# Kernel optimization log

Measured on AMD Instinct MI355X. Metric: run time of the kernel, lower is better.

The kernel has to match this reference:

```python
import jax, jax.numpy as jnp
import numpy as np

B, T_ENC, E, T_DEC, N_MELS, H, A = 32, 256, 512, 200, 80, 1024, 128


def setup_inputs() -> dict:
    key = jax.random.key(0)
    ks = jax.random.split(key, 20)
    rn = lambda k, s, sc: (jax.random.normal(k, s, jnp.float32) * sc)
    return {
        "inputs": rn(ks[0], (B, T_ENC, E), 1.0),
        "padded_mels": rn(ks[1], (B, N_MELS, T_DEC), 1.0),
        "W_enc": rn(ks[2], (E, A), 0.04),
        "W_q": rn(ks[3], (H, A), 0.03),
        "conv_w": rn(ks[4], (32, 1, 31), 0.18),
        "conv_b": jnp.zeros((32,), jnp.float32),
        "W_loc": rn(ks[5], (32, A), 0.18),
        "v_e": rn(ks[6], (A,), 0.09),
        "pw1": rn(ks[7], (N_MELS, 256), 0.11),
        "pb1": jnp.zeros((256,), jnp.float32),
        "pw2": rn(ks[8], (256, 256), 0.06),
        "pb2": jnp.zeros((256,), jnp.float32),
        "Wi1": rn(ks[9], (256 + E, 4 * H), 0.03),
        "Wh1": rn(ks[10], (H, 4 * H), 0.03),
        "bl1": jnp.zeros((4 * H,), jnp.float32),
        "Wi2": rn(ks[11], (H, 4 * H), 0.03),
        "Wh2": rn(ks[12], (H, 4 * H), 0.03),
        "bl2": jnp.zeros((4 * H,), jnp.float32),
        "Wp": rn(ks[13], (H + E, N_MELS), 0.025),
        "bp": jnp.zeros((N_MELS,), jnp.float32),
    }


def _lstm_cell(x, h, c, Wi, Wh, b):
    g = x @ Wi + h @ Wh + b
    i, f, gg, o = jnp.split(g, 4, axis=-1)
    c = jax.nn.sigmoid(f) * c + jax.nn.sigmoid(i) * jnp.tanh(gg)
    h = jax.nn.sigmoid(o) * jnp.tanh(c)
    return h, c


def reference(inputs, padded_mels, W_enc, W_q, conv_w, conv_b, W_loc, v_e,
              pw1, pb1, pw2, pb2, Wi1, Wh1, bl1, Wi2, Wh2, bl2, Wp, bp):
    b, t_enc, e = inputs.shape
    n_mels, t_dec = padded_mels.shape[1], padded_mels.shape[2]
    proc_enc = inputs @ W_enc  # [B, T_enc, A]
    # teacher forcing: prepend go frame, use frames 0..T_dec-1 as inputs
    go = jnp.zeros((b, n_mels, 1), inputs.dtype)
    prev_mels = jnp.moveaxis(jnp.concatenate([go, padded_mels], axis=-1)[:, :, :-1], -1, 0)  # [T_dec,B,80]

    def step(carry, prev_mel):
        h1, c1, h2, c2, ctx, aw_cum = carry
        # prenet (dropout omitted: eval/deterministic reference)
        x = jax.nn.relu(prev_mel @ pw1 + pb1)
        x = jax.nn.relu(x @ pw2 + pb2)
        # 2-layer LSTM on [prenet, prev context]
        lstm_in = jnp.concatenate([x, ctx], axis=-1)
        h1n, c1n = _lstm_cell(lstm_in, h1, c1, Wi1, Wh1, bl1)
        h2n, c2n = _lstm_cell(h1n, h2, c2, Wi2, Wh2, bl2)
        # location-sensitive attention
        q = h2n @ W_q  # [B, A]
        loc = jax.lax.conv_general_dilated(aw_cum[:, None, :], conv_w, (1,), "SAME",
                                           dimension_numbers=("NCH", "OIH", "NCH"))
        loc = loc + conv_b[None, :, None]
        loc = jnp.swapaxes(loc, 1, 2) @ W_loc  # [B, T_enc, A]
        energies = jnp.tanh(q[:, None, :] + loc + proc_enc) @ v_e  # [B, T_enc]
        aw = jax.nn.softmax(energies, axis=1)
        ctx_n = jnp.einsum("bt,bte->be", aw, inputs)
        out = jnp.concatenate([h2n, ctx_n], axis=-1) @ Wp + bp  # [B, 80]
        return (h1n, c1n, h2n, c2n, ctx_n, aw_cum + aw), out

    z = lambda *s: jnp.zeros(s, inputs.dtype)
    carry0 = (z(b, H), z(b, H), z(b, H), z(b, H), z(b, e), z(b, t_enc))
    _, mels = jax.lax.scan(step, carry0, prev_mels)
    return mels  # [T_dec, B, 80]
```

## Files before the change

### kernel.cpp

```cpp
#include <hip/hip_runtime.h>
#include <hip/hip_fp16.h>

#define BB   32
#define TENC 256
#define EE   512
#define TDEC 200
#define NM   80
#define HH   1024
#define AA   128
#define GG   4096
#define K1   1792
#define K2   2048

#define NGRP  16
#define GRPSZ 16

typedef _Float16 h8v  __attribute__((ext_vector_type(8)));
typedef float    f32x4 __attribute__((ext_vector_type(4)));

__device__ __forceinline__ float sigf(float x){ return 1.0f/(1.0f + __expf(-x)); }
__device__ __forceinline__ float tanhfast(float x){ return 1.0f - 2.0f/(1.0f + __expf(2.0f*x)); }

__device__ __forceinline__ unsigned short h2b(float f){
    _Float16 h = (_Float16)f; unsigned short u; __builtin_memcpy(&u, &h, 2); return u;
}
__device__ __forceinline__ void st64(unsigned long long* p, unsigned long long v){
    __hip_atomic_store(p, v, __ATOMIC_RELAXED, __HIP_MEMORY_SCOPE_AGENT);
}
__device__ __forceinline__ void st32(unsigned int* p, unsigned int v){
    __hip_atomic_store(p, v, __ATOMIC_RELAXED, __HIP_MEMORY_SCOPE_AGENT);
}
__device__ __forceinline__ unsigned long long ld64(const unsigned long long* p){
    return __hip_atomic_load(p, __ATOMIC_RELAXED, __HIP_MEMORY_SCOPE_AGENT);
}
__device__ __forceinline__ unsigned int ld32(const unsigned int* p){
    return __hip_atomic_load(p, __ATOMIC_RELAXED, __HIP_MEMORY_SCOPE_AGENT);
}


__global__ void k_zero(float* __restrict__ p, int n){
    int i = blockIdx.x*blockDim.x + threadIdx.x;
    if(i < n) p[i] = 0.f;
}

__global__ void k_cvt_half(const float* __restrict__ src, __half* __restrict__ dst, int n){
    int i = blockIdx.x*blockDim.x + threadIdx.x;
    int stride = gridDim.x*blockDim.x;
    for(; i<n; i+=stride) dst[i] = __float2half(src[i]);
}

__global__ __launch_bounds__(256) void k_transpose2(const float* __restrict__ src,
                                                    _Float16* __restrict__ dst,
                                                    int K, int C, int dstStride, int kOff, int pack){
    __shared__ float tile[32][33];
    const int tid = threadIdx.x;
    const int c0 = blockIdx.x*32, k0 = blockIdx.y*32;
    const int cl = tid & 31, r8 = tid >> 5;
    #pragma unroll
    for(int i=0;i<4;i++){
        const int k = k0 + r8 + i*8;
        if(k < K && c0+cl < C) tile[r8 + i*8][cl] = src[(size_t)k*C + c0 + cl];
    }
    __syncthreads();
    const int kl = tid & 31, c8 = tid >> 5;
    #pragma unroll
    for(int i=0;i<4;i++){
        const int c = c0 + c8 + i*8;
        if(c < C && k0+kl < K){
            const int p = pack ? ((c & 1023)*4 + (c >> 10)) : c;
            dst[(size_t)p*dstStride + kOff + k0 + kl] = (_Float16)tile[kl][c8 + i*8];
        }
    }
}

__global__ __launch_bounds__(256) void k_wfrag(const _Float16* __restrict__ WT,
                                               _Float16* __restrict__ WF, int K){
    const int tid = threadIdx.x;
    const int l = tid & 63, f = tid >> 6;
    const int ct = blockIdx.y;
    const int kc = blockIdx.x*4 + f;
    const h8v v = *(const h8v*)(WT + (size_t)(ct*16 + (l & 15))*K + kc*32 + ((l >> 4) << 3));
    *(h8v*)(WF + ((size_t)(ct*(K >> 5) + kc)*64 + l)*8) = v;
}

__global__ __launch_bounds__(128) void k_proc_enc(const float* __restrict__ inputs,
                                                  const float* __restrict__ Wenc,
                                                  __half* __restrict__ pe_h){
    const int row = blockIdx.x;
    const int a   = threadIdx.x;
    const float* in = inputs + (size_t)row*EE;
    float acc = 0.f;
    for(int k=0;k<EE;k++) acc = fmaf(in[k], Wenc[k*AA + a], acc);
    pe_h[(size_t)row*AA + a] = __float2half(acc);
}

__global__ __launch_bounds__(320) void k_pip(const float* __restrict__ inputs,
                                             const float* __restrict__ Wp_c,
                                             __half* __restrict__ PIP){
    const int b = blockIdx.x >> 6, t4 = (blockIdx.x & 63)*4;
    __shared__ float xs[4*EE];
    const int tid = threadIdx.x;
    for(int i=tid; i<4*EE; i+=320) xs[i] = inputs[((size_t)b*TENC + t4)*EE + i];
    __syncthreads();
    const int tl = tid/80, m = tid%80;
    float acc = 0.f;
    for(int k=0;k<EE;k++) acc = fmaf(xs[tl*EE + k], Wp_c[k*NM + m], acc);
    PIP[((size_t)b*TENC + t4 + tl)*NM + m] = __float2half(acc);
}

__global__ __launch_bounds__(256) void k_prenet(const float* __restrict__ pmels,
                                                const float* __restrict__ pw1, const float* __restrict__ pb1,
                                                const float* __restrict__ pw2, const float* __restrict__ pb2,
                                                _Float16* __restrict__ XS1h){
    const int t = blockIdx.x;
    __shared__ float pm[BB*NM];
    __shared__ float h1s[BB*256];
    const int tid = threadIdx.x;
    for(int el=tid; el<BB*NM; el+=256){
        const int b = el/NM, m = el%NM;
        pm[el] = (t==0) ? 0.f : pmels[(size_t)(b*NM + m)*TDEC + (t-1)];
    }
    __syncthreads();
    const int a = tid;
    float acc[BB];
    #pragma unroll
    for(int b=0;b<BB;b++) acc[b]=0.f;
    for(int m=0;m<NM;m++){
        const float w = pw1[m*256 + a];
        #pragma unroll
        for(int b=0;b<BB;b++) acc[b] = fmaf(pm[b*NM+m], w, acc[b]);
    }
    {
        const float bias = pb1[a];
        for(int b=0;b<BB;b++) h1s[b*256+a] = fmaxf(acc[b]+bias, 0.f);
    }
    __syncthreads();
    #pragma unroll
    for(int b=0;b<BB;b++) acc[b]=0.f;
    for(int k=0;k<256;k++){
        const float w = pw2[k*256 + a];
        #pragma unroll
        for(int b=0;b<BB;b++) acc[b] = fmaf(h1s[b*256+k], w, acc[b]);
    }
    {
        const float bias = pb2[a];
        #pragma unroll
        for(int b=0;b<BB;b++)
            XS1h[((size_t)t*BB + b)*K1 + a] = (_Float16)fmaxf(acc[b]+bias, 0.f);
    }
}

__global__ void k_mloc(const float* __restrict__ conv_w, const float* __restrict__ conv_b,
                       const float* __restrict__ W_loc, float* __restrict__ Mloc, float* __restrict__ cbp){
    const int a = threadIdx.x;
    for(int d=0; d<31; d++){
        float s = 0.f;
        for(int ch=0; ch<32; ch++) s = fmaf(conv_w[ch*31 + d], W_loc[ch*AA + a], s);
        Mloc[d*AA + a] = s;
    }
    float s = 0.f;
    for(int ch=0; ch<32; ch++) s = fmaf(conv_b[ch], W_loc[ch*AA + a], s);
    cbp[a] = s;
}


__device__ __forceinline__ void gridbar(unsigned int* bb, unsigned int bi, int tid, int bid, int& dead){
    __syncthreads();
    if(tid == 0){
        const int g = bid >> 4;
        unsigned int v = __hip_atomic_fetch_add(&bb[g*32], 1u, __ATOMIC_RELAXED, __HIP_MEMORY_SCOPE_AGENT);
        if(v == bi*GRPSZ - 1u){
            unsigned int w = __hip_atomic_fetch_add(&bb[512], 1u, __ATOMIC_RELAXED, __HIP_MEMORY_SCOPE_AGENT);
            if(w == bi*NGRP - 1u)
                st32(&bb[544], bi);
        }
        if(!dead){
            unsigned int guard = 0;
            if((bid & 15) == 0){
                while(ld32(&bb[544]) < bi){
                    __builtin_amdgcn_s_sleep(4);
                    if(++guard > 3000000u){ dead = 1; break; }
                }
                #pragma unroll
                for(int m=1; m<GRPSZ; m++) st32(&bb[576 + (bid+m)*32], bi);
            } else {
                while(ld32(&bb[576 + bid*32]) < bi){
                    __builtin_amdgcn_s_sleep(4);
                    if(++guard > 3000000u){ dead = 1; break; }
                }
            }
        }
    }
    __syncthreads();
}

template<int K, bool SC1>
__device__ __forceinline__ void lstm_phase(
    const _Float16* __restrict__ XSh, const _Float16* __restrict__ WF,
    const float* __restrict__ bias, float& cv,
    _Float16* hA, int strideA, int offA,
    _Float16* hB, int strideB, int offB,
    float* part, float* stage, int tid, int bid)
{
    constexpr int KCN = K/256;
    const int l = tid & 63, kw = tid >> 6;
    f32x4 accL = {0.f,0.f,0.f,0.f}, accH = {0.f,0.f,0.f,0.f};
    const int r = l & 15;
    const _Float16* aptr = XSh + (size_t)r*K + (size_t)kw*KCN*32 + ((l >> 4) << 3);
    const _Float16* bptr = WF + ((size_t)(bid*(K >> 5) + kw*KCN)*64 + l)*8;
    #pragma unroll
    for(int kc=0; kc<KCN; kc++){
        const h8v b8 = *(const h8v*)(bptr + (size_t)kc*512);
        h8v aL, aH;
        if constexpr(SC1){
            union { unsigned long long u[2]; h8v v; } uL, uH;
            const unsigned long long* pL = (const unsigned long long*)(aptr + (size_t)kc*32);
            const unsigned long long* pH = (const unsigned long long*)(aptr + (size_t)16*K + (size_t)kc*32);
            uL.u[0] = ld64(pL);   uL.u[1] = ld64(pL+1);
            uH.u[0] = ld64(pH);   uH.u[1] = ld64(pH+1);
            aL = uL.v; aH = uH.v;
        } else {
            aL = *(const h8v*)(aptr + (size_t)kc*32);
            aH = *(const h8v*)(aptr + (size_t)16*K + (size_t)kc*32);
        }
        accL = __builtin_amdgcn_mfma_f32_16x16x32_f16(aL, b8, accL, 0, 0, 0);
        accH = __builtin_amdgcn_mfma_f32_16x16x32_f16(aH, b8, accH, 0, 0, 0);
    }
    {
        const int r0 = (l >> 4) << 2, c = l & 15;
        #pragma unroll
        for(int j=0;j<4;j++){
            part[(kw*32 + r0 + j)*18 + c]      = accL[j];
            part[(kw*32 + 16 + r0 + j)*18 + c] = accH[j];
        }
    }
    __syncthreads();
    if(tid < 128){
        const int b = tid & 31, cl = tid >> 5;
        float g[4];
        #pragma unroll
        for(int gi=0; gi<4; gi++){
            const int c2 = cl*4 + gi;
            float s = 0.f;
            #pragma unroll
            for(int q=0;q<8;q++) s += part[(q*32 + b)*18 + c2];
            const int p = bid*16 + c2;
            g[gi] = s + bias[(p & 3)*HH + (p >> 2)];
        }
        const float cn = sigf(g[1])*cv + sigf(g[0])*tanhfast(g[2]);
        cv = cn;
        stage[tid] = sigf(g[3])*tanhfast(cn);
    }
    __syncthreads();
    if(tid < 32){
        const int b = tid;
        unsigned long long pk =
              (unsigned long long)h2b(stage[0*32+b])
            | ((unsigned long long)h2b(stage[1*32+b]) << 16)
            | ((unsigned long long)h2b(stage[2*32+b]) << 32)
            | ((unsigned long long)h2b(stage[3*32+b]) << 48);
        st64((unsigned long long*)hA + ((size_t)b*strideA + offA + bid*4)/4, pk);
        if(hB) st64((unsigned long long*)hB + ((size_t)b*strideB + offB + bid*4)/4, pk);
    }
}

__global__ __launch_bounds__(512) void k_decode(
    _Float16* __restrict__ XS1h, _Float16* __restrict__ XS2h,
    const _Float16* __restrict__ W1F, const _Float16* __restrict__ W2F,
    const float* __restrict__ bl1, const float* __restrict__ bl2,
    const _Float16* __restrict__ WqT, const float* __restrict__ cbp,
    const float* __restrict__ Mloc, const float* __restrict__ ve,
    const __half* __restrict__ pe,
    const __half* __restrict__ inputs_h, const __half* __restrict__ PIP,
    const _Float16* __restrict__ WohT, const float* __restrict__ bp,
    float* __restrict__ out, unsigned int* __restrict__ bar)
{
    const int tid = threadIdx.x, bid = blockIdx.x;

    __shared__ float s_ml[31*AA];
    __shared__ float s_ves[AA];
    __shared__ float s_part[8*32*18];
    __shared__ float s_h2s[1024];
    __shared__ float s_qc[4*AA];
    __shared__ float s_qf[AA];
    __shared__ float s_awin[288];
    __shared__ float s_aw[TENC];
    __shared__ float s_awc[TENC];
    __shared__ float s_red1[320];
    __shared__ float s_red2[320];
    __shared__ float s_sred[8];

    for(int i=tid; i<31*AA; i+=512) s_ml[i] = Mloc[i];
    if(tid < AA) s_ves[tid] = ve[tid];
    if(bid < BB) for(int i=tid; i<TENC; i+=512) s_awc[i] = 0.f;
    __syncthreads();

    float c1v = 0.f, c2v = 0.f;
    int dead = 0;
    unsigned int bi = 0;

    for(int t=0; t<TDEC; t++){
        const int p = t & 1;
        const _Float16* x1c = XS1h + (size_t)t*BB*K1;
        _Float16* x1n = XS1h + (size_t)(t+1)*BB*K1;
        _Float16* x2p = XS2h + (size_t)p*BB*K2;
        _Float16* x2n = XS2h + (size_t)(1-p)*BB*K2;

        lstm_phase<K1,false>(x1c, W1F, bl1, c1v,
                             x2p, K2, 0,
                             x1n, K1, 768,
                             s_part, s_qf, tid, bid);
        gridbar(bar, ++bi, tid, bid, dead);

        lstm_phase<K2,true>(x2p, W2F, bl2, c2v,
                            x2n, K2, 1024,
                            (_Float16*)nullptr, 0, 0,
                            s_part, s_qf, tid, bid);
        gridbar(bar, ++bi, tid, bid, dead);

        if(bid < BB){
            const int b = bid;
            {
                const unsigned int* hp = (const unsigned int*)(x2n + (size_t)b*K2 + 1024);
                union { unsigned int u; _Float16 h[2]; } cu;
                cu.u = ld32(hp + tid);
                s_h2s[2*tid]   = (float)cu.h[0];
                s_h2s[2*tid+1] = (float)cu.h[1];
            }
            for(int i=tid; i<286; i+=512){
                const int g = i - 15;
                s_awin[i] = (g>=0 && g<TENC) ? s_awc[g] : 0.f;
            }
            __syncthreads();
            {
                const int a = tid & 127, tp = tid >> 7;
                float qa = 0.f;
                const _Float16* wq = WqT + (size_t)a*HH + tp*256;
                const float* hs = s_h2s + tp*256;
                for(int kb=0; kb<256; kb+=8){
                    const h8v w8 = *(const h8v*)(wq + kb);
                    #pragma unroll
                    for(int i2=0;i2<8;i2++) qa = fmaf((float)w8[i2], hs[kb+i2], qa);
                }
                s_qc[tp*AA + a] = qa;
            }
            __syncthreads();
            if(tid < AA) s_qf[tid] = s_qc[tid] + s_qc[AA+tid] + s_qc[2*AA+tid] + s_qc[3*AA+tid] + cbp[tid];
            __syncthreads();
            float* s_ep = s_part;
            #pragma unroll
            for(int it=0; it<2; it++){
                const int ti = tid & 255, ah = (tid >> 8) + 2*it;
                const int a0 = ah*32;
                float s[32];
                const h8v* pp = (const h8v*)((const _Float16*)pe + ((size_t)(b*TENC + ti))*AA + a0);
                #pragma unroll
                for(int vq=0; vq<4; vq++){
                    const h8v pv = pp[vq];
                    #pragma unroll
                    for(int j=0;j<8;j++) s[vq*8+j] = s_qf[a0+vq*8+j] + (float)pv[j];
                }
                for(int d=0; d<31; d++){
                    const float w = s_awin[ti+d];
                    #pragma unroll
                    for(int j=0;j<32;j++) s[j] = fmaf(w, s_ml[d*AA + a0 + j], s[j]);
                }
                float es = 0.f;
                #pragma unroll
                for(int j=0;j<32;j++) es = fmaf(tanhfast(s[j]), s_ves[a0+j], es);
                s_ep[ah*256 + ti] = es;
            }
            __syncthreads();
            float e = -1e30f;
            if(tid < 256) e = s_ep[tid] + s_ep[256+tid] + s_ep[512+tid] + s_ep[768+tid];
            float m_ = e;
            #pragma unroll
            for(int o=32;o>=1;o>>=1) m_ = fmaxf(m_, __shfl_xor(m_, o));
            if((tid&63)==0 && tid<256) s_sred[tid>>6] = m_;
            __syncthreads();
            const float mm = fmaxf(fmaxf(s_sred[0],s_sred[1]), fmaxf(s_sred[2],s_sred[3]));
            const float pv2 = (tid<256) ? __expf(e - mm) : 0.f;
            float sum = pv2;
            #pragma unroll
            for(int o=32;o>=1;o>>=1) sum += __shfl_xor(sum, o);
            if((tid&63)==0 && tid<256) s_sred[4+(tid>>6)] = sum;
            __syncthreads();
            sum = s_sred[4]+s_sred[5]+s_sred[6]+s_sred[7];
            if(tid < 256){
                const float awv = pv2/sum;
                s_aw[tid] = awv;
                s_awc[tid] += awv;
            }
            __syncthreads();
            float* ctxred = s_part;
            {
                const int ch8 = tid & 63, tq = tid >> 6;
                const _Float16* ib = (const _Float16*)inputs_h + (size_t)b*TENC*EE + ch8*8;
                float a_[8];
                #pragma unroll
                for(int j=0;j<8;j++) a_[j]=0.f;
                for(int tt=tq; tt<TENC; tt+=8){
                    const float wv = s_aw[tt];
                    const h8v x8 = *(const h8v*)(ib + (size_t)tt*EE);
                    #pragma unroll
                    for(int j=0;j<8;j++) a_[j] = fmaf(wv, (float)x8[j], a_[j]);
                }
                #pragma unroll
                for(int j=0;j<8;j++) ctxred[tq*512 + ch8*8 + j] = a_[j];
            }
            __syncthreads();
            if(tid < 256){
                const int ch = 2*tid;
                float s0=0.f, s1=0.f;
                #pragma unroll
                for(int q=0;q<8;q++){ s0 += ctxred[q*512 + ch]; s1 += ctxred[q*512 + ch + 1]; }
                union { unsigned int u; _Float16 h[2]; } cu;
                cu.h[0] = (_Float16)s0; cu.h[1] = (_Float16)s1;
                st32((unsigned int*)(x1n + (size_t)b*K1 + 256) + tid, cu.u);
            }
            if(tid < 320){
                const int m2 = tid % 80, kh = tid / 80;
                float s1 = 0.f;
                const _Float16* wo = WohT + (size_t)m2*HH + kh*256;
                const float* hs = s_h2s + kh*256;
                for(int kb=0; kb<256; kb+=8){
                    const h8v w8 = *(const h8v*)(wo + kb);
                    #pragma unroll
                    for(int i2=0;i2<8;i2++) s1 = fmaf((float)w8[i2], hs[kb+i2], s1);
                }
                s_red1[kh*80 + m2] = s1;
                float s2 = 0.f;
                const __half* pp2 = PIP + ((size_t)(b*TENC) + kh*64)*NM + m2;
                const float* awp = s_aw + kh*64;
                for(int tt=0; tt<64; tt++)
                    s2 = fmaf(awp[tt], __half2float(pp2[(size_t)tt*NM]), s2);
                s_red2[kh*80 + m2] = s2;
            }
            __syncthreads();
            if(tid < NM){
                const float o = s_red1[tid]+s_red1[80+tid]+s_red1[160+tid]+s_red1[240+tid]
                              + s_red2[tid]+s_red2[80+tid]+s_red2[160+tid]+s_red2[240+tid] + bp[tid];
                out[((size_t)t*BB + b)*NM + tid] = o;
            }
        }
        gridbar(bar, ++bi, tid, bid, dead);
    }
}


extern "C" void kernel_launch(void* const* d_in, const int* in_sizes, int n_in,
                              void* d_out, int out_size, void* d_ws, size_t ws_size,
                              hipStream_t stream)
{
    const float* inputs = (const float*)d_in[0];
    const float* pmels  = (const float*)d_in[1];
    const float* W_enc  = (const float*)d_in[2];
    const float* W_q    = (const float*)d_in[3];
    const float* conv_w = (const float*)d_in[4];
    const float* conv_b = (const float*)d_in[5];
    const float* W_loc  = (const float*)d_in[6];
    const float* v_e    = (const float*)d_in[7];
    const float* pw1    = (const float*)d_in[8];
    const float* pb1    = (const float*)d_in[9];
    const float* pw2    = (const float*)d_in[10];
    const float* pb2    = (const float*)d_in[11];
    const float* Wi1    = (const float*)d_in[12];
    const float* Wh1    = (const float*)d_in[13];
    const float* bl1    = (const float*)d_in[14];
    const float* Wi2    = (const float*)d_in[15];
    const float* Wh2    = (const float*)d_in[16];
    const float* bl2    = (const float*)d_in[17];
    const float* Wp     = (const float*)d_in[18];
    const float* bp     = (const float*)d_in[19];
    float* out = (float*)d_out;
    (void)in_sizes; (void)n_in; (void)out_size; (void)ws_size;

    char* ws = (char*)d_ws;
    size_t off = 0;
    auto carve = [&](size_t bytes)->char* {
        char* p = ws + off;
        off += (bytes + 255) & ~(size_t)255;
        return p;
    };
    __half*    inputs_h = (__half*)   carve((size_t)BB*TENC*EE*2);
    __half*    pe_h     = (__half*)   carve((size_t)BB*TENC*AA*2);
    __half*    PIP      = (__half*)   carve((size_t)BB*TENC*NM*2);
    _Float16*  XS1h     = (_Float16*) carve((size_t)(TDEC+1)*BB*K1*2);
    _Float16*  XS2h     = (_Float16*) carve((size_t)2*BB*K2*2);
    _Float16*  WA       = (_Float16*) carve((size_t)GG*K2*2);
    _Float16*  WB       = (_Float16*) carve((size_t)GG*K1*2);
    _Float16*  W2F      = (_Float16*) carve((size_t)GG*K2*2);
    _Float16*  WqT      = (_Float16*) carve((size_t)AA*HH*2);
    _Float16*  WohT     = (_Float16*) carve((size_t)NM*HH*2);
    const int NBAR = 576 + 256*32;
    unsigned int* bar   = (unsigned int*)carve((size_t)NBAR*4);
    float* Mloc = (float*)carve((size_t)31*AA*4);
    float* cbp  = (float*)carve((size_t)AA*4);
    _Float16* W1F = WA;

    k_zero<<<(NBAR+255)/256,256,0,stream>>>((float*)bar, NBAR);
    k_zero<<<(2*BB*K2/2+255)/256,256,0,stream>>>((float*)XS2h, 2*BB*K2/2);
    k_zero<<<(BB*K1/2+255)/256,256,0,stream>>>((float*)XS1h, BB*K1/2);
    k_cvt_half<<<2048,256,0,stream>>>(inputs, inputs_h, BB*TENC*EE);
    k_proc_enc<<<BB*TENC,128,0,stream>>>(inputs, W_enc, pe_h);
    k_prenet<<<TDEC,256,0,stream>>>(pmels, pw1,pb1,pw2,pb2, XS1h);
    k_mloc<<<1,128,0,stream>>>(conv_w, conv_b, W_loc, Mloc, cbp);
    k_transpose2<<<dim3(GG/32, 1024/32),256,0,stream>>>(Wi2, WA, 1024, GG, K2, 0,    1);
    k_transpose2<<<dim3(GG/32, 1024/32),256,0,stream>>>(Wh2, WA, 1024, GG, K2, 1024, 1);
    k_wfrag<<<dim3(K2/128, GG/16),256,0,stream>>>(WA, W2F, K2);
    k_transpose2<<<dim3(GG/32,  768/32),256,0,stream>>>(Wi1, WB, 768,  GG, K1, 0,    1);
    k_transpose2<<<dim3(GG/32, 1024/32),256,0,stream>>>(Wh1, WB, 1024, GG, K1, 768,  1);
    k_wfrag<<<dim3(K1/128, GG/16),256,0,stream>>>(WB, W1F, K1);
    k_transpose2<<<dim3(AA/32, 1024/32),256,0,stream>>>(W_q, WqT, 1024, AA, HH, 0,   0);
    k_transpose2<<<dim3(3,     1024/32),256,0,stream>>>(Wp,  WohT, 1024, NM, HH, 0,  0);
    k_pip<<<BB*64,320,0,stream>>>(inputs, Wp + (size_t)HH*NM, PIP);

    {
        void* ka[17];
        ka[0]  = (void*)&XS1h;
        ka[1]  = (void*)&XS2h;
        ka[2]  = (void*)&W1F;
        ka[3]  = (void*)&W2F;
        ka[4]  = (void*)&bl1;
        ka[5]  = (void*)&bl2;
        ka[6]  = (void*)&WqT;
        ka[7]  = (void*)&cbp;
        ka[8]  = (void*)&Mloc;
        ka[9]  = (void*)&v_e;
        ka[10] = (void*)&pe_h;
        ka[11] = (void*)&inputs_h;
        ka[12] = (void*)&PIP;
        ka[13] = (void*)&WohT;
        ka[14] = (void*)&bp;
        ka[15] = (void*)&out;
        ka[16] = (void*)&bar;
        hipLaunchCooperativeKernel((const void*)k_decode, dim3(256), dim3(512),
                                   ka, 0, stream);
    }
}
```

Before: 11.97 ms.

## Precompute LSTM partial GEMMs off the critical path and simplify grid barrier

Splits each LSTM gate GEMM into K-windows. The parts whose inputs are already known (prenet, h1, h2 recurrent terms) are accumulated right after the second barrier of the previous step, overlapping the attention work of the first 32 blocks. Only the context window (layer 1) and the fresh h1 window (layer 2) are computed between barriers, which shortens the serialized chain per step. h2 now lives in a separate ping-pong buffer instead of the combined XS2 layout. The grid barrier also drops the separate release flag: the group leader polls the level-2 counter directly, and the sleep interval is halved. In exchange, more accumulator registers stay live across the attention phase.

```diff
diff --git a/kernel.cpp b/kernel.cpp
--- a/kernel.cpp
+++ b/kernel.cpp
@@ -169,23 +169,20 @@
     if(tid == 0){
         const int g = bid >> 4;
         unsigned int v = __hip_atomic_fetch_add(&bb[g*32], 1u, __ATOMIC_RELAXED, __HIP_MEMORY_SCOPE_AGENT);
-        if(v == bi*GRPSZ - 1u){
-            unsigned int w = __hip_atomic_fetch_add(&bb[512], 1u, __ATOMIC_RELAXED, __HIP_MEMORY_SCOPE_AGENT);
-            if(w == bi*NGRP - 1u)
-                st32(&bb[544], bi);
-        }
+        if(v == bi*GRPSZ - 1u)
+            __hip_atomic_fetch_add(&bb[512], 1u, __ATOMIC_RELAXED, __HIP_MEMORY_SCOPE_AGENT);
         if(!dead){
             unsigned int guard = 0;
             if((bid & 15) == 0){
-                while(ld32(&bb[544]) < bi){
-                    __builtin_amdgcn_s_sleep(4);
+                while(ld32(&bb[512]) < bi*NGRP){
+                    __builtin_amdgcn_s_sleep(2);
                     if(++guard > 3000000u){ dead = 1; break; }
                 }
                 #pragma unroll
                 for(int m=1; m<GRPSZ; m++) st32(&bb[576 + (bid+m)*32], bi);
             } else {
                 while(ld32(&bb[576 + bid*32]) < bi){
-                    __builtin_amdgcn_s_sleep(4);
+                    __builtin_amdgcn_s_sleep(2);
                     if(++guard > 3000000u){ dead = 1; break; }
                 }
             }
@@ -194,38 +191,39 @@
     __syncthreads();
 }
 
-template<int K, bool SC1>
-__device__ __forceinline__ void lstm_phase(
-    const _Float16* __restrict__ XSh, const _Float16* __restrict__ WF,
-    const float* __restrict__ bias, float& cv,
-    _Float16* hA, int strideA, int offA,
-    _Float16* hB, int strideB, int offB,
-    float* part, float* stage, int tid, int bid)
+template<int LF, bool AGENT>
+__device__ __forceinline__ void gemm_win(f32x4& accL, f32x4& accH,
+    const _Float16* __restrict__ aCol, int strideA,
+    const _Float16* __restrict__ bWave, int l)
 {
-    constexpr int KCN = K/256;
-    const int l = tid & 63, kw = tid >> 6;
-    f32x4 accL = {0.f,0.f,0.f,0.f}, accH = {0.f,0.f,0.f,0.f};
     const int r = l & 15;
-    const _Float16* aptr = XSh + (size_t)r*K + (size_t)kw*KCN*32 + ((l >> 4) << 3);
-    const _Float16* bptr = WF + ((size_t)(bid*(K >> 5) + kw*KCN)*64 + l)*8;
+    const _Float16* a0 = aCol + (size_t)r*strideA + ((l >> 4) << 3);
     #pragma unroll
-    for(int kc=0; kc<KCN; kc++){
-        const h8v b8 = *(const h8v*)(bptr + (size_t)kc*512);
+    for(int j=0;j<LF;j++){
+        const h8v b8 = *(const h8v*)(bWave + (size_t)j*512);
         h8v aL, aH;
-        if constexpr(SC1){
+        if constexpr(AGENT){
             union { unsigned long long u[2]; h8v v; } uL, uH;
-            const unsigned long long* pL = (const unsigned long long*)(aptr + (size_t)kc*32);
-            const unsigned long long* pH = (const unsigned long long*)(aptr + (size_t)16*K + (size_t)kc*32);
+            const unsigned long long* pL = (const unsigned long long*)(a0 + j*32);
+            const unsigned long long* pH = (const unsigned long long*)(a0 + (size_t)16*strideA + j*32);
             uL.u[0] = ld64(pL);   uL.u[1] = ld64(pL+1);
             uH.u[0] = ld64(pH);   uH.u[1] = ld64(pH+1);
             aL = uL.v; aH = uH.v;
         } else {
-            aL = *(const h8v*)(aptr + (size_t)kc*32);
-            aH = *(const h8v*)(aptr + (size_t)16*K + (size_t)kc*32);
+            aL = *(const h8v*)(a0 + j*32);
+            aH = *(const h8v*)(a0 + (size_t)16*strideA + j*32);
         }
         accL = __builtin_amdgcn_mfma_f32_16x16x32_f16(aL, b8, accL, 0, 0, 0);
         accH = __builtin_amdgcn_mfma_f32_16x16x32_f16(aH, b8, accH, 0, 0, 0);
     }
+}
+
+__device__ __forceinline__ void lstm_finish(
+    const f32x4& accL, const f32x4& accH,
+    const float* __restrict__ bias, float& cv,
+    _Float16* __restrict__ hDst, int strideH,
+    float* part, float* stage, int tid, int bid, int l, int kw)
+{
     {
         const int r0 = (l >> 4) << 2, c = l & 15;
         #pragma unroll
@@ -259,13 +257,12 @@
             | ((unsigned long long)h2b(stage[1*32+b]) << 16)
             | ((unsigned long long)h2b(stage[2*32+b]) << 32)
             | ((unsigned long long)h2b(stage[3*32+b]) << 48);
-        st64((unsigned long long*)hA + ((size_t)b*strideA + offA + bid*4)/4, pk);
-        if(hB) st64((unsigned long long*)hB + ((size_t)b*strideB + offB + bid*4)/4, pk);
+        st64((unsigned long long*)(hDst + (size_t)b*strideH + bid*4), pk);
     }
 }
 
 __global__ __launch_bounds__(512) void k_decode(
-    _Float16* __restrict__ XS1h, _Float16* __restrict__ XS2h,
+    _Float16* __restrict__ XS1h, _Float16* __restrict__ H2P,
     const _Float16* __restrict__ W1F, const _Float16* __restrict__ W2F,
     const float* __restrict__ bl1, const float* __restrict__ bl2,
     const _Float16* __restrict__ WqT, const float* __restrict__ cbp,
@@ -276,6 +273,7 @@
     float* __restrict__ out, unsigned int* __restrict__ bar)
 {
     const int tid = threadIdx.x, bid = blockIdx.x;
+    const int l = tid & 63, kw = tid >> 6;
 
     __shared__ float s_ml[31*AA];
     __shared__ float s_ves[AA];
@@ -299,37 +297,50 @@
     int dead = 0;
     unsigned int bi = 0;
 
+    const f32x4 z4 = {0.f,0.f,0.f,0.f};
+    f32x4 p1L = z4, p1H = z4;
+    f32x4 p2L = z4, p2H = z4;
+
+    gemm_win<1,false>(p1L,p1H, XS1h + kw*32,        K1, W1F + ((size_t)(bid*56 + kw)*64 + l)*8, l);
+    gemm_win<4,false>(p1L,p1H, XS1h + 768 + kw*128, K1, W1F + ((size_t)(bid*56 + 24 + kw*4)*64 + l)*8, l);
+    gemm_win<4,true >(p2L,p2H, H2P + (size_t)BB*HH + kw*128, HH, W2F + ((size_t)(bid*64 + 32 + kw*4)*64 + l)*8, l);
+
     for(int t=0; t<TDEC; t++){
-        const int p = t & 1;
-        const _Float16* x1c = XS1h + (size_t)t*BB*K1;
-        _Float16* x1n = XS1h + (size_t)(t+1)*BB*K1;
-        _Float16* x2p = XS2h + (size_t)p*BB*K2;
-        _Float16* x2n = XS2h + (size_t)(1-p)*BB*K2;
-
-        lstm_phase<K1,false>(x1c, W1F, bl1, c1v,
-                             x2p, K2, 0,
-                             x1n, K1, 768,
-                             s_part, s_qf, tid, bid);
+        _Float16* rowT  = XS1h + (size_t)t*BB*K1;
+        _Float16* rowT1 = XS1h + (size_t)(t+1)*BB*K1;
+        _Float16* h2cur = H2P + (size_t)(t & 1)*BB*HH;
+
+        {
+            f32x4 aL = p1L, aH = p1H;
+            gemm_win<2,false>(aL,aH, rowT + 256 + kw*64, K1, W1F + ((size_t)(bid*56 + 8 + kw*2)*64 + l)*8, l);
+            lstm_finish(aL,aH, bl1, c1v, rowT1 + 768, K1, s_part, s_qf, tid, bid, l, kw);
+        }
         gridbar(bar, ++bi, tid, bid, dead);
 
-        lstm_phase<K2,true>(x2p, W2F, bl2, c2v,
-                            x2n, K2, 1024,
-                            (_Float16*)nullptr, 0, 0,
-                            s_part, s_qf, tid, bid);
+        {
+            f32x4 aL = p2L, aH = p2H;
+            gemm_win<4,false>(aL,aH, rowT1 + 768 + kw*128, K1, W2F + ((size_t)(bid*64 + kw*4)*64 + l)*8, l);
+            lstm_finish(aL,aH, bl2, c2v, h2cur, HH, s_part, s_qf, tid, bid, l, kw);
+        }
         gridbar(bar, ++bi, tid, bid, dead);
+
+        p1L = z4; p1H = z4; p2L = z4; p2H = z4;
+        gemm_win<1,false>(p1L,p1H, rowT1 + kw*32,        K1, W1F + ((size_t)(bid*56 + kw)*64 + l)*8, l);
+        gemm_win<4,false>(p1L,p1H, rowT1 + 768 + kw*128, K1, W1F + ((size_t)(bid*56 + 24 + kw*4)*64 + l)*8, l);
+        gemm_win<4,true >(p2L,p2H, h2cur + kw*128,       HH, W2F + ((size_t)(bid*64 + 32 + kw*4)*64 + l)*8, l);
 
         if(bid < BB){
             const int b = bid;
             {
-                const unsigned int* hp = (const unsigned int*)(x2n + (size_t)b*K2 + 1024);
+                const unsigned int* hp = (const unsigned int*)(h2cur + (size_t)b*HH);
                 union { unsigned int u; _Float16 h[2]; } cu;
                 cu.u = ld32(hp + tid);
                 s_h2s[2*tid]   = (float)cu.h[0];
                 s_h2s[2*tid+1] = (float)cu.h[1];
             }
             for(int i=tid; i<286; i+=512){
-                const int g = i - 15;
-                s_awin[i] = (g>=0 && g<TENC) ? s_awc[g] : 0.f;
+                const int g2 = i - 15;
+                s_awin[i] = (g2>=0 && g2<TENC) ? s_awc[g2] : 0.f;
             }
             __syncthreads();
             {
@@ -416,7 +427,7 @@
                 for(int q=0;q<8;q++){ s0 += ctxred[q*512 + ch]; s1 += ctxred[q*512 + ch + 1]; }
                 union { unsigned int u; _Float16 h[2]; } cu;
                 cu.h[0] = (_Float16)s0; cu.h[1] = (_Float16)s1;
-                st32((unsigned int*)(x1n + (size_t)b*K1 + 256) + tid, cu.u);
+                st32((unsigned int*)(rowT1 + (size_t)b*K1 + 256) + tid, cu.u);
             }
             if(tid < 320){
                 const int m2 = tid % 80, kh = tid / 80;
@@ -486,7 +497,7 @@
     __half*    pe_h     = (__half*)   carve((size_t)BB*TENC*AA*2);
     __half*    PIP      = (__half*)   carve((size_t)BB*TENC*NM*2);
     _Float16*  XS1h     = (_Float16*) carve((size_t)(TDEC+1)*BB*K1*2);
-    _Float16*  XS2h     = (_Float16*) carve((size_t)2*BB*K2*2);
+    _Float16*  H2P      = (_Float16*) carve((size_t)2*BB*HH*2);
     _Float16*  WA       = (_Float16*) carve((size_t)GG*K2*2);
     _Float16*  WB       = (_Float16*) carve((size_t)GG*K1*2);
     _Float16*  W2F      = (_Float16*) carve((size_t)GG*K2*2);
@@ -499,7 +510,7 @@
     _Float16* W1F = WA;
 
     k_zero<<<(NBAR+255)/256,256,0,stream>>>((float*)bar, NBAR);
-    k_zero<<<(2*BB*K2/2+255)/256,256,0,stream>>>((float*)XS2h, 2*BB*K2/2);
+    k_zero<<<(2*BB*HH/2+255)/256,256,0,stream>>>((float*)H2P, 2*BB*HH/2);
     k_zero<<<(BB*K1/2+255)/256,256,0,stream>>>((float*)XS1h, BB*K1/2);
     k_cvt_half<<<2048,256,0,stream>>>(inputs, inputs_h, BB*TENC*EE);
     k_proc_enc<<<BB*TENC,128,0,stream>>>(inputs, W_enc, pe_h);
@@ -518,7 +529,7 @@
     {
         void* ka[17];
         ka[0]  = (void*)&XS1h;
-        ka[1]  = (void*)&XS2h;
+        ka[1]  = (void*)&H2P;
         ka[2]  = (void*)&W1F;
         ka[3]  = (void*)&W2F;
         ka[4]  = (void*)&bl1;
```

After: 11.36 ms. -5.1%, faster.
